# Kernel tuning notes

Hardware: AMD Instinct MI355X
Metric: run time of the kernel (lower is better)

Reference implementation:

```python
import jax, jax.numpy as jnp
import numpy as np

B, T, C = 1, 2048, 1024
H, D = 16, 64  # n_head, head_size (n_query_groups == n_head -> plain MHA)


def build_rope_cache(seq_len, n_elem, base=10000):
    theta = 1.0 / (base ** (jnp.arange(0, n_elem, 2, dtype=jnp.float32) / n_elem))
    idx_theta = jnp.outer(jnp.arange(seq_len, dtype=jnp.float32), theta)
    idx_theta = jnp.concatenate([idx_theta, idx_theta], axis=-1)  # torch .repeat(1, 2)
    return jnp.cos(idx_theta), jnp.sin(idx_theta)


def apply_rope(x, cos, sin):
    d = x.shape[-1]
    x1, x2 = x[..., : d // 2], x[..., d // 2 :]
    rotated = jnp.concatenate([-x2, x1], axis=-1)
    return x * cos + rotated * sin


def fastmax_attention(q, k, v):
    """Fastmax: first-order Taylor approx of softmax attention, causal, O(n*d^2).
    score(i,j) = 1 + q_i . k_j (temperature=1, zero RPE, no dropout);
    out_i = sum_{j<=i} score*v_j / sum_{j<=i} score, via causal cumulative sums."""
    n = q.shape[2]
    kcum = jnp.cumsum(k, axis=2)                                       # (B,H,T,D)
    kvcum = jnp.cumsum(jnp.einsum('bhnd,bhne->bhnde', k, v), axis=2)   # (B,H,T,D,D)
    den = jnp.arange(1, n + 1, dtype=q.dtype) + jnp.einsum('bhnd,bhnd->bhn', q, kcum)
    num = jnp.cumsum(v, axis=2) + jnp.einsum('bhnd,bhnde->bhne', q, kvcum)
    return num / den[..., None]


def setup_inputs() -> dict:
    key = jax.random.key(0)
    k1, k2, k3 = jax.random.split(key, 3)
    scale = 0.02
    x = jax.random.normal(k1, (B, T, C), dtype=jnp.float32)
    w_attn = jax.random.normal(k2, (3 * H * D, C), dtype=jnp.float32) * scale
    w_proj = jax.random.normal(k3, (C, H * D), dtype=jnp.float32) * scale
    cos, sin = build_rope_cache(T, D)
    return {"x": x, "w_attn": w_attn, "w_proj": w_proj, "cos": cos, "sin": sin}


def reference(x, w_attn, w_proj, cos, sin):
    Bx, Tx, Cx = x.shape
    qkv = x @ w_attn.T                                  # (B,T,3HD)
    qkv = qkv.reshape(Bx, Tx, H, 3, D).transpose(0, 2, 3, 1, 4)  # (B,H,3,T,D)
    q, k, v = qkv[:, :, 0], qkv[:, :, 1], qkv[:, :, 2]
    q = apply_rope(q, cos, sin)
    k = apply_rope(k, cos, sin)
    y = fastmax_attention(q, k, v)                      # (B,H,T,D)
    y = y.transpose(0, 2, 1, 3).reshape(Bx, Tx, H * D)
    return y @ w_proj.T
```

## Files before the change

kernel.cpp:

```cpp
#include <hip/hip_runtime.h>

#define T_LEN 2048
#define C_DIM 1024
#define H_NUM 16
#define D_DIM 64
#define QKV_N (3 * H_NUM * D_DIM)
#define L_CHK 64
#define NC (T_LEN / L_CHK)

typedef _Float16 h8 __attribute__((ext_vector_type(8)));
typedef _Float16 h4 __attribute__((ext_vector_type(4)));
typedef float f32x4 __attribute__((ext_vector_type(4)));

__global__ __launch_bounds__(256) void split3_f16(
    const float* __restrict__ x, _Float16* __restrict__ xh,
    _Float16* __restrict__ xl, const float* __restrict__ wa,
    _Float16* __restrict__ wah, _Float16* __restrict__ wal,
    const float* __restrict__ wp, _Float16* __restrict__ wph) {
  int i = (blockIdx.x * 256 + threadIdx.x) * 8;
  const float* src;
  _Float16 *dh, *dl = nullptr;
  int base;
  if (i < 2097152) {
    src = x; dh = xh; dl = xl; base = i;
  } else if (i < 2097152 + 3145728) {
    src = wa; dh = wah; dl = wal; base = i - 2097152;
  } else {
    src = wp; dh = wph; base = i - 5242880;
  }
  float4 a = *(const float4*)(src + base);
  float4 b = *(const float4*)(src + base + 4);
  float v[8] = {a.x, a.y, a.z, a.w, b.x, b.y, b.z, b.w};
  h8 hv, lv;
#pragma unroll
  for (int j = 0; j < 8; ++j) {
    float s = v[j] * 64.f;
    _Float16 h = (_Float16)s;
    hv[j] = h;
    lv[j] = (_Float16)(s - (float)h);
  }
  *(h8*)(dh + base) = hv;
  if (dl) *(h8*)(dl + base) = lv;
}

template <int BN, bool ROPE, bool SPLIT3>
__global__ __launch_bounds__(256) void gemm_nt_f16(
    const _Float16* __restrict__ Ah, const _Float16* __restrict__ Al,
    const _Float16* __restrict__ Bh, const _Float16* __restrict__ Bl,
    float* __restrict__ C, const float* __restrict__ cosb,
    const float* __restrict__ sinb, float* __restrict__ qout,
    float* __restrict__ kout, float* __restrict__ vout, int M, int N, int K,
    float outscale) {
  constexpr int NJ = BN / 32;
  constexpr int NARR = SPLIT3 ? 2 : 1;
  constexpr int GEMM_BYTES = (64 * 64 * 2 + BN * 64 * 2) * NARR;
  constexpr int ROPE_BYTES = ROPE ? (2 * 64 * 64 * 4) : 0;
  constexpr int SMEM_BYTES = GEMM_BYTES > ROPE_BYTES ? GEMM_BYTES : ROPE_BYTES;
  __shared__ __align__(16) char smem[SMEM_BYTES];
  _Float16* sAh = (_Float16*)smem;
  _Float16* sAl = sAh + 64 * 64;
  _Float16* sBh = sAh + 64 * 64 * NARR;
  _Float16* sBl = sBh + BN * 64;
  const int tid = threadIdx.x;
  const int wave = tid >> 6;
  const int lane = tid & 63;
  const int bm = blockIdx.y * 64;
  const int bn = blockIdx.x * BN;
  const int wm = wave >> 1;
  const int wn = wave & 1;
  const int srow = lane >> 3;
  const int sblk = ((lane & 7) ^ srow) * 8;
  const int quad = lane >> 4;
  const int lrow = lane & 15;

  f32x4 acc[2][NJ];
#pragma unroll
  for (int i = 0; i < 2; ++i)
#pragma unroll
    for (int j = 0; j < NJ; ++j) acc[i][j] = (f32x4){0.f, 0.f, 0.f, 0.f};

  for (int k0 = 0; k0 < K; k0 += 64) {
#pragma unroll
    for (int it = 0; it < 2; ++it) {
      const int ch = wave + it * 4;
      const int row = ch * 8 + srow;
      const _Float16* ga = Ah + (size_t)(bm + row) * K + k0 + sblk;
      __builtin_amdgcn_global_load_lds(
          (const __attribute__((address_space(1))) void*)ga,
          (__attribute__((address_space(3))) void*)(sAh + ch * 512), 16, 0, 0);
      if constexpr (SPLIT3) {
        const _Float16* gb = Al + (size_t)(bm + row) * K + k0 + sblk;
        __builtin_amdgcn_global_load_lds(
            (const __attribute__((address_space(1))) void*)gb,
            (__attribute__((address_space(3))) void*)(sAl + ch * 512), 16, 0,
            0);
      }
    }
#pragma unroll
    for (int it = 0; it < BN / 32; ++it) {
      const int ch = wave + it * 4;
      const int row = ch * 8 + srow;
      const _Float16* ga = Bh + (size_t)(bn + row) * K + k0 + sblk;
      __builtin_amdgcn_global_load_lds(
          (const __attribute__((address_space(1))) void*)ga,
          (__attribute__((address_space(3))) void*)(sBh + ch * 512), 16, 0, 0);
      if constexpr (SPLIT3) {
        const _Float16* gb = Bl + (size_t)(bn + row) * K + k0 + sblk;
        __builtin_amdgcn_global_load_lds(
            (const __attribute__((address_space(1))) void*)gb,
            (__attribute__((address_space(3))) void*)(sBl + ch * 512), 16, 0,
            0);
      }
    }
    __syncthreads();
#pragma unroll
    for (int kk = 0; kk < 2; ++kk) {
      h8 ah[2], al[2], bh[NJ], bl[NJ];
#pragma unroll
      for (int i = 0; i < 2; ++i) {
        const int row = wm * 32 + i * 16 + lrow;
        const int ra = row * 64 + (((kk * 4 + quad) ^ (row & 7)) * 8);
        ah[i] = *(const h8*)&sAh[ra];
        if constexpr (SPLIT3) al[i] = *(const h8*)&sAl[ra];
      }
#pragma unroll
      for (int j = 0; j < NJ; ++j) {
        const int row = wn * (BN / 2) + j * 16 + lrow;
        const int rb = row * 64 + (((kk * 4 + quad) ^ (row & 7)) * 8);
        bh[j] = *(const h8*)&sBh[rb];
        if constexpr (SPLIT3) bl[j] = *(const h8*)&sBl[rb];
      }
#pragma unroll
      for (int i = 0; i < 2; ++i)
#pragma unroll
        for (int j = 0; j < NJ; ++j) {
          acc[i][j] = __builtin_amdgcn_mfma_f32_16x16x32_f16(
              ah[i], bh[j], acc[i][j], 0, 0, 0);
          if constexpr (SPLIT3) {
            acc[i][j] = __builtin_amdgcn_mfma_f32_16x16x32_f16(
                ah[i], bl[j], acc[i][j], 0, 0, 0);
            acc[i][j] = __builtin_amdgcn_mfma_f32_16x16x32_f16(
                al[i], bh[j], acc[i][j], 0, 0, 0);
          }
        }
    }
    __syncthreads();
  }
  if constexpr (!ROPE) {
#pragma unroll
    for (int i = 0; i < 2; ++i) {
      const int rbase = bm + wm * 32 + i * 16 + quad * 4;
#pragma unroll
      for (int j = 0; j < NJ; ++j) {
        const int col = bn + wn * (BN / 2) + j * 16 + lrow;
#pragma unroll
        for (int r = 0; r < 4; ++r)
          C[(size_t)(rbase + r) * N + col] = acc[i][j][r] * outscale;
      }
    }
  } else {
    float* cs = (float*)smem;
    float* sn = cs + 4096;
#pragma unroll
    for (int m = 0; m < 4; ++m) {
      int el = (tid + m * 256) * 4;
      *(float4*)&cs[el] = *(const float4*)&cosb[bm * D_DIM + el];
      *(float4*)&sn[el] = *(const float4*)&sinb[bm * D_DIM + el];
    }
    __syncthreads();
    const int colbase = bn + wn * 64;
    const int type = (colbase >> 6) % 3;
    const int head = colbase / 192;
    float* dst = (type == 0) ? qout : (type == 1) ? kout : vout;
    const size_t hbase = (size_t)head * T_LEN * D_DIM;
#pragma unroll
    for (int i = 0; i < 2; ++i) {
      const int tloc0 = wm * 32 + i * 16 + quad * 4;
#pragma unroll
      for (int r = 0; r < 4; ++r) {
        const int tloc = tloc0 + r;
        float* trow = dst + hbase + (size_t)(bm + tloc) * D_DIM;
#pragma unroll
        for (int j = 0; j < NJ; ++j) {
          const int d = j * 16 + lrow;
          float val = acc[i][j][r] * outscale;
          if (type < 2) {
            float rotv = ((j < 2) ? -acc[i][j + 2][r] : acc[i][j - 2][r]) *
                         outscale;
            val = val * cs[tloc * D_DIM + d] + rotv * sn[tloc * D_DIM + d];
          }
          trow[d] = val;
        }
      }
    }
  }
}

__global__ __launch_bounds__(256) void chunk_kv(
    const float* __restrict__ k, const float* __restrict__ v,
    float* __restrict__ kvchunk, float* __restrict__ kschunk,
    float* __restrict__ vschunk) {
  __shared__ float Ks[L_CHK][D_DIM];
  __shared__ float Vs[L_CHK][D_DIM];
  int blk = blockIdx.x;
  const size_t off = ((size_t)(blk / NC) * T_LEN + (blk % NC) * L_CHK) * D_DIM;
  int tid = threadIdx.x;
#pragma unroll
  for (int m = 0; m < 4; ++m) {
    int el = (tid + m * 256) * 4;
    *(float4*)&((float*)Ks)[el] = *(const float4*)&k[off + el];
    *(float4*)&((float*)Vs)[el] = *(const float4*)&v[off + el];
  }
  __syncthreads();
  int e = tid & 63;
  int q2 = tid >> 6;
  float acc[16] = {};
  for (int t = 0; t < L_CHK; ++t) {
    float ve = Vs[t][e];
#pragma unroll
    for (int m = 0; m < 16; ++m) acc[m] += Ks[t][q2 * 16 + m] * ve;
  }
  float* outb = kvchunk + (size_t)blk * (D_DIM * D_DIM);
#pragma unroll
  for (int m = 0; m < 16; ++m) outb[(q2 * 16 + m) * D_DIM + e] = acc[m];
  if (tid < 64) {
    float s = 0.f;
    for (int t = 0; t < L_CHK; ++t) s += Ks[t][tid];
    kschunk[(size_t)blk * D_DIM + tid] = s;
  } else if (tid < 128) {
    float s = 0.f;
    for (int t = 0; t < L_CHK; ++t) s += Vs[t][tid - 64];
    vschunk[(size_t)blk * D_DIM + (tid - 64)] = s;
  }
}

__global__ __launch_bounds__(256) void scan_fused(
    const float* __restrict__ kvchunk, float* __restrict__ kvpref,
    const float* __restrict__ kschunk, const float* __restrict__ vschunk,
    float* __restrict__ kspref, float* __restrict__ vspref) {
  int b = blockIdx.x;
  int tid = threadIdx.x;
  if (b < 256) {
    int gid = b * 256 + tid;
    int h = gid >> 12;
    int de = gid & 4095;
    float vals[NC];
#pragma unroll
    for (int c = 0; c < NC; ++c)
      vals[c] = kvchunk[((size_t)(h * NC + c) << 12) + de];
    float run = 0.f;
#pragma unroll
    for (int c = 0; c < NC; ++c) {
      kvpref[((size_t)(h * NC + c) << 12) + de] = run;
      run += vals[c];
    }
  } else {
    int gid = (b - 256) * 256 + tid;
    int h = gid >> 6, d = gid & 63;
    float kv_[NC], vv_[NC];
#pragma unroll
    for (int c = 0; c < NC; ++c) {
      size_t idx = (size_t)(h * NC + c) * 64 + d;
      kv_[c] = kschunk[idx];
      vv_[c] = vschunk[idx];
    }
    float rk = 0.f, rv = 0.f;
#pragma unroll
    for (int c = 0; c < NC; ++c) {
      size_t idx = (size_t)(h * NC + c) * 64 + d;
      kspref[idx] = rk;
      vspref[idx] = rv;
      rk += kv_[c];
      rv += vv_[c];
    }
  }
}

__global__ __launch_bounds__(256) void attn_out(
    const float* __restrict__ q, const float* __restrict__ k,
    const float* __restrict__ v, const float* __restrict__ kvpref,
    const float* __restrict__ kspref, const float* __restrict__ vspref,
    _Float16* __restrict__ yh) {
  __shared__ float Ks[L_CHK * D_DIM];
  __shared__ float Vs[L_CHK * D_DIM];
  __shared__ float Ss[L_CHK][L_CHK + 1];
  int blk = blockIdx.x;
  int h = blk / NC, c = blk % NC;
  int tid = threadIdx.x;
  int r = tid & 63;
  int g = tid >> 6;
  const size_t off = ((size_t)h * T_LEN + c * L_CHK) * D_DIM;
#pragma unroll
  for (int m = 0; m < 4; ++m) {
    int el = (tid + m * 256) * 4;
    *(float4*)&Ks[el] = *(const float4*)&k[off + el];
    *(float4*)&Vs[el] = *(const float4*)&v[off + el];
  }
  float qv[D_DIM];
#pragma unroll
  for (int i = 0; i < 16; ++i) {
    float4 t4 = *(const float4*)&q[off + r * D_DIM + i * 4];
    qv[i * 4 + 0] = t4.x; qv[i * 4 + 1] = t4.y;
    qv[i * 4 + 2] = t4.z; qv[i * 4 + 3] = t4.w;
  }
  __syncthreads();
#pragma unroll
  for (int jj = 0; jj < 16; ++jj) {
    int j = g * 16 + jj;
    const float4* krow = (const float4*)&Ks[j * D_DIM];
    float sdot = 0.f;
#pragma unroll
    for (int i = 0; i < 16; ++i) {
      float4 kj = krow[i];
      sdot += qv[i * 4] * kj.x + qv[i * 4 + 1] * kj.y + qv[i * 4 + 2] * kj.z +
              qv[i * 4 + 3] * kj.w;
    }
    Ss[r][j] = (j <= r) ? (sdot + 1.f) : 0.f;
  }
  __syncthreads();
  const float* kvp = kvpref + (size_t)blk * (D_DIM * D_DIM);
#pragma unroll
  for (int m = 0; m < 4; ++m) {
    int el = (tid + m * 256) * 4;
    *(float4*)&Ks[el] = *(const float4*)&kvp[el];
  }
  __syncthreads();
  const float* ksp = kspref + (size_t)blk * D_DIM;
  const float* vsp = vspref + (size_t)blk * D_DIM;
  float den = (float)(c * L_CHK);
#pragma unroll
  for (int i = 0; i < 16; ++i) {
    float4 kk = *(const float4*)&ksp[i * 4];
    den += qv[i * 4] * kk.x + qv[i * 4 + 1] * kk.y + qv[i * 4 + 2] * kk.z +
           qv[i * 4 + 3] * kk.w;
  }
  float4 num[4];
#pragma unroll
  for (int i = 0; i < 4; ++i) num[i] = *(const float4*)&vsp[g * 16 + i * 4];
#pragma unroll
  for (int d = 0; d < D_DIM; ++d) {
    float qd = qv[d];
    const float4* kvrow = (const float4*)&Ks[d * D_DIM + g * 16];
#pragma unroll
    for (int i = 0; i < 4; ++i) {
      float4 k4 = kvrow[i];
      num[i].x += qd * k4.x; num[i].y += qd * k4.y;
      num[i].z += qd * k4.z; num[i].w += qd * k4.w;
    }
  }
  float rs = 0.f;
#pragma unroll 8
  for (int j = 0; j < L_CHK; ++j) {
    float f = Ss[r][j];
    rs += f;
    const float4* vrow = (const float4*)&Vs[j * D_DIM + g * 16];
#pragma unroll
    for (int i = 0; i < 4; ++i) {
      float4 v4 = vrow[i];
      num[i].x += f * v4.x; num[i].y += f * v4.y;
      num[i].z += f * v4.z; num[i].w += f * v4.w;
    }
  }
  den += rs;
  float inv = 1.f / den;
  int t = c * L_CHK + r;
  size_t ybase = (size_t)t * (H_NUM * D_DIM) + h * D_DIM + g * 16;
#pragma unroll
  for (int i = 0; i < 4; ++i) {
    h4 hv;
    hv[0] = (_Float16)(num[i].x * inv);
    hv[1] = (_Float16)(num[i].y * inv);
    hv[2] = (_Float16)(num[i].z * inv);
    hv[3] = (_Float16)(num[i].w * inv);
    *(h4*)&yh[ybase + i * 4] = hv;
  }
}

extern "C" void kernel_launch(void* const* d_in, const int* in_sizes, int n_in,
                              void* d_out, int out_size, void* d_ws,
                              size_t ws_size, hipStream_t stream) {
  const float* x = (const float*)d_in[0];
  const float* w_attn = (const float*)d_in[1];
  const float* w_proj = (const float*)d_in[2];
  const float* cosb = (const float*)d_in[3];
  const float* sinb = (const float*)d_in[4];
  float* out = (float*)d_out;

  char* ws = (char*)d_ws;
  float* kvchunk = (float*)ws;
  float* kvpref = (float*)(ws + 8388608);
  float* qbuf = (float*)(ws + 25165824);
  float* kbuf = (float*)(ws + 25165824 + 8388608);
  float* vbuf = (float*)(ws + 25165824 + 16777216);
  _Float16* xh = (_Float16*)(ws + 50331648);
  _Float16* xl = (_Float16*)(ws + 50331648 + 4194304);
  _Float16* yh = (_Float16*)(ws + 50331648);
  _Float16* wah = (_Float16*)(ws + 58720256);
  _Float16* wal = (_Float16*)(ws + 58720256 + 6291456);
  float* kschunk = (float*)(ws + 58720256);
  float* vschunk = (float*)(ws + 58720256 + 131072);
  float* kspref = (float*)(ws + 58720256 + 262144);
  float* vspref = (float*)(ws + 58720256 + 393216);
  _Float16* wph = (_Float16*)(ws + 71303168);

  split3_f16<<<3072, 256, 0, stream>>>(x, xh, xl, w_attn, wah, wal, w_proj,
                                       wph);

  {
    dim3 grid(QKV_N / 128, T_LEN / 64);
    gemm_nt_f16<128, true, true><<<grid, 256, 0, stream>>>(
        xh, xl, wah, wal, nullptr, cosb, sinb, qbuf, kbuf, vbuf, T_LEN, QKV_N,
        C_DIM, 1.f / 4096.f);
  }
  chunk_kv<<<H_NUM * NC, 256, 0, stream>>>(kbuf, vbuf, kvchunk, kschunk,
                                           vschunk);
  scan_fused<<<260, 256, 0, stream>>>(kvchunk, kvpref, kschunk, vschunk,
                                      kspref, vspref);
  attn_out<<<H_NUM * NC, 256, 0, stream>>>(qbuf, kbuf, vbuf, kvpref, kspref,
                                           vspref, yh);
  {
    dim3 grid(C_DIM / 64, T_LEN / 64);
    gemm_nt_f16<64, false, false><<<grid, 256, 0, stream>>>(
        yh, nullptr, wph, nullptr, out, nullptr, nullptr, nullptr, nullptr,
        nullptr, T_LEN, C_DIM, C_DIM, 1.f / 64.f);
  }
}
```

Baseline: 172.2 us.

## Fuse chunk KV, prefix scan and attention output into one flag-synchronized kernel

Merges the per-chunk K^T V computation, the cross-chunk prefix scan and the attention output into a single kernel. Each block publishes its chunk state, then sets a release flag, and later blocks spin on the flags of earlier chunks of the same head before summing their states directly. This removes two kernel launches and the kvpref round trip through global memory. In exchange, later chunks do O(c) redundant reads of earlier chunk states, and the code relies on all 512 blocks being co-resident or scheduled in order so the spin-waits cannot deadlock.

```diff
diff --git a/kernel.cpp b/kernel.cpp
--- a/kernel.cpp
+++ b/kernel.cpp
@@ -16,7 +16,15 @@
     const float* __restrict__ x, _Float16* __restrict__ xh,
     _Float16* __restrict__ xl, const float* __restrict__ wa,
     _Float16* __restrict__ wah, _Float16* __restrict__ wal,
-    const float* __restrict__ wp, _Float16* __restrict__ wph) {
+    const float* __restrict__ wp, _Float16* __restrict__ wph,
+    int* __restrict__ flags) {
+  if (blockIdx.x == 0) {
+    int t = threadIdx.x;
+    __hip_atomic_store(&flags[t], 0, __ATOMIC_RELEASE,
+                       __HIP_MEMORY_SCOPE_AGENT);
+    __hip_atomic_store(&flags[t + 256], 0, __ATOMIC_RELEASE,
+                       __HIP_MEMORY_SCOPE_AGENT);
+  }
   int i = (blockIdx.x * 256 + threadIdx.x) * 8;
   const float* src;
   _Float16 *dh, *dl = nullptr;
@@ -196,99 +204,21 @@
   }
 }
 
-__global__ __launch_bounds__(256) void chunk_kv(
-    const float* __restrict__ k, const float* __restrict__ v,
-    float* __restrict__ kvchunk, float* __restrict__ kschunk,
-    float* __restrict__ vschunk) {
-  __shared__ float Ks[L_CHK][D_DIM];
-  __shared__ float Vs[L_CHK][D_DIM];
-  int blk = blockIdx.x;
-  const size_t off = ((size_t)(blk / NC) * T_LEN + (blk % NC) * L_CHK) * D_DIM;
-  int tid = threadIdx.x;
-#pragma unroll
-  for (int m = 0; m < 4; ++m) {
-    int el = (tid + m * 256) * 4;
-    *(float4*)&((float*)Ks)[el] = *(const float4*)&k[off + el];
-    *(float4*)&((float*)Vs)[el] = *(const float4*)&v[off + el];
-  }
-  __syncthreads();
-  int e = tid & 63;
-  int q2 = tid >> 6;
-  float acc[16] = {};
-  for (int t = 0; t < L_CHK; ++t) {
-    float ve = Vs[t][e];
-#pragma unroll
-    for (int m = 0; m < 16; ++m) acc[m] += Ks[t][q2 * 16 + m] * ve;
-  }
-  float* outb = kvchunk + (size_t)blk * (D_DIM * D_DIM);
-#pragma unroll
-  for (int m = 0; m < 16; ++m) outb[(q2 * 16 + m) * D_DIM + e] = acc[m];
-  if (tid < 64) {
-    float s = 0.f;
-    for (int t = 0; t < L_CHK; ++t) s += Ks[t][tid];
-    kschunk[(size_t)blk * D_DIM + tid] = s;
-  } else if (tid < 128) {
-    float s = 0.f;
-    for (int t = 0; t < L_CHK; ++t) s += Vs[t][tid - 64];
-    vschunk[(size_t)blk * D_DIM + (tid - 64)] = s;
-  }
-}
-
-__global__ __launch_bounds__(256) void scan_fused(
-    const float* __restrict__ kvchunk, float* __restrict__ kvpref,
-    const float* __restrict__ kschunk, const float* __restrict__ vschunk,
-    float* __restrict__ kspref, float* __restrict__ vspref) {
-  int b = blockIdx.x;
-  int tid = threadIdx.x;
-  if (b < 256) {
-    int gid = b * 256 + tid;
-    int h = gid >> 12;
-    int de = gid & 4095;
-    float vals[NC];
-#pragma unroll
-    for (int c = 0; c < NC; ++c)
-      vals[c] = kvchunk[((size_t)(h * NC + c) << 12) + de];
-    float run = 0.f;
-#pragma unroll
-    for (int c = 0; c < NC; ++c) {
-      kvpref[((size_t)(h * NC + c) << 12) + de] = run;
-      run += vals[c];
-    }
-  } else {
-    int gid = (b - 256) * 256 + tid;
-    int h = gid >> 6, d = gid & 63;
-    float kv_[NC], vv_[NC];
-#pragma unroll
-    for (int c = 0; c < NC; ++c) {
-      size_t idx = (size_t)(h * NC + c) * 64 + d;
-      kv_[c] = kschunk[idx];
-      vv_[c] = vschunk[idx];
-    }
-    float rk = 0.f, rv = 0.f;
-#pragma unroll
-    for (int c = 0; c < NC; ++c) {
-      size_t idx = (size_t)(h * NC + c) * 64 + d;
-      kspref[idx] = rk;
-      vspref[idx] = rv;
-      rk += kv_[c];
-      rv += vv_[c];
-    }
-  }
-}
-
-__global__ __launch_bounds__(256) void attn_out(
+__global__ __launch_bounds__(256) void attn_fused(
     const float* __restrict__ q, const float* __restrict__ k,
-    const float* __restrict__ v, const float* __restrict__ kvpref,
-    const float* __restrict__ kspref, const float* __restrict__ vspref,
-    _Float16* __restrict__ yh) {
+    const float* __restrict__ v, float* __restrict__ kvchunk,
+    float* __restrict__ kschunk, float* __restrict__ vschunk,
+    int* __restrict__ flags, _Float16* __restrict__ yh) {
   __shared__ float Ks[L_CHK * D_DIM];
   __shared__ float Vs[L_CHK * D_DIM];
   __shared__ float Ss[L_CHK][L_CHK + 1];
-  int blk = blockIdx.x;
-  int h = blk / NC, c = blk % NC;
-  int tid = threadIdx.x;
-  int r = tid & 63;
-  int g = tid >> 6;
+  __shared__ float sKp[D_DIM];
+  __shared__ float sVp[D_DIM];
+  const int blk = blockIdx.x;
+  const int h = blk / NC, c = blk % NC;
+  const int tid = threadIdx.x;
+  const int r = tid & 63;
+  const int g = tid >> 6;
   const size_t off = ((size_t)h * T_LEN + c * L_CHK) * D_DIM;
 #pragma unroll
   for (int m = 0; m < 4; ++m) {
@@ -304,6 +234,32 @@
     qv[i * 4 + 2] = t4.z; qv[i * 4 + 3] = t4.w;
   }
   __syncthreads();
+  {
+    float agg[16] = {};
+    for (int t = 0; t < L_CHK; ++t) {
+      float ve = Vs[t * D_DIM + r];
+#pragma unroll
+      for (int m = 0; m < 16; ++m)
+        agg[m] += Ks[t * D_DIM + g * 16 + m] * ve;
+    }
+    float* outb = kvchunk + (size_t)blk * (D_DIM * D_DIM);
+#pragma unroll
+    for (int m = 0; m < 16; ++m) outb[(g * 16 + m) * D_DIM + r] = agg[m];
+    if (tid < 64) {
+      float s = 0.f;
+      for (int t = 0; t < L_CHK; ++t) s += Ks[t * D_DIM + tid];
+      kschunk[blk * D_DIM + tid] = s;
+    } else if (tid < 128) {
+      float s = 0.f;
+      for (int t = 0; t < L_CHK; ++t) s += Vs[t * D_DIM + (tid - 64)];
+      vschunk[blk * D_DIM + (tid - 64)] = s;
+    }
+  }
+  __threadfence();
+  __syncthreads();
+  if (tid == 0)
+    __hip_atomic_store(&flags[blk], 1, __ATOMIC_RELEASE,
+                       __HIP_MEMORY_SCOPE_AGENT);
 #pragma unroll
   for (int jj = 0; jj < 16; ++jj) {
     int j = g * 16 + jj;
@@ -318,25 +274,51 @@
     Ss[r][j] = (j <= r) ? (sdot + 1.f) : 0.f;
   }
   __syncthreads();
-  const float* kvp = kvpref + (size_t)blk * (D_DIM * D_DIM);
+  f32x4 pacc[4];
+#pragma unroll
+  for (int m = 0; m < 4; ++m) pacc[m] = (f32x4){0.f, 0.f, 0.f, 0.f};
+  float kp = 0.f, vp = 0.f;
+  if (c > 0) {
+    if (tid == 0) {
+      for (int cc = 0; cc < c; ++cc)
+        while (__hip_atomic_load(&flags[h * NC + cc], __ATOMIC_ACQUIRE,
+                                 __HIP_MEMORY_SCOPE_AGENT) == 0) {
+        }
+    }
+    __syncthreads();
+    for (int cc = 0; cc < c; ++cc) {
+      const float* src = kvchunk + (size_t)(h * NC + cc) * (D_DIM * D_DIM);
+#pragma unroll
+      for (int m = 0; m < 4; ++m) {
+        int el = (tid + m * 256) * 4;
+        pacc[m] += *(const f32x4*)&src[el];
+      }
+      if (tid < 64)
+        kp += kschunk[(h * NC + cc) * D_DIM + tid];
+      else if (tid < 128)
+        vp += vschunk[(h * NC + cc) * D_DIM + (tid - 64)];
+    }
+  }
 #pragma unroll
   for (int m = 0; m < 4; ++m) {
     int el = (tid + m * 256) * 4;
-    *(float4*)&Ks[el] = *(const float4*)&kvp[el];
-  }
+    *(f32x4*)&Ks[el] = pacc[m];
+  }
+  if (tid < 64)
+    sKp[tid] = kp;
+  else if (tid < 128)
+    sVp[tid - 64] = vp;
   __syncthreads();
-  const float* ksp = kspref + (size_t)blk * D_DIM;
-  const float* vsp = vspref + (size_t)blk * D_DIM;
   float den = (float)(c * L_CHK);
 #pragma unroll
   for (int i = 0; i < 16; ++i) {
-    float4 kk = *(const float4*)&ksp[i * 4];
+    const float4 kk = *(const float4*)&sKp[i * 4];
     den += qv[i * 4] * kk.x + qv[i * 4 + 1] * kk.y + qv[i * 4 + 2] * kk.z +
            qv[i * 4 + 3] * kk.w;
   }
   float4 num[4];
 #pragma unroll
-  for (int i = 0; i < 4; ++i) num[i] = *(const float4*)&vsp[g * 16 + i * 4];
+  for (int i = 0; i < 4; ++i) num[i] = *(const float4*)&sVp[g * 16 + i * 4];
 #pragma unroll
   for (int d = 0; d < D_DIM; ++d) {
     float qd = qv[d];
@@ -388,7 +370,9 @@
 
   char* ws = (char*)d_ws;
   float* kvchunk = (float*)ws;
-  float* kvpref = (float*)(ws + 8388608);
+  float* kschunk = (float*)(ws + 8388608);
+  float* vschunk = (float*)(ws + 8519680);
+  int* flags = (int*)(ws + 8650752);
   float* qbuf = (float*)(ws + 25165824);
   float* kbuf = (float*)(ws + 25165824 + 8388608);
   float* vbuf = (float*)(ws + 25165824 + 16777216);
@@ -397,14 +381,10 @@
   _Float16* yh = (_Float16*)(ws + 50331648);
   _Float16* wah = (_Float16*)(ws + 58720256);
   _Float16* wal = (_Float16*)(ws + 58720256 + 6291456);
-  float* kschunk = (float*)(ws + 58720256);
-  float* vschunk = (float*)(ws + 58720256 + 131072);
-  float* kspref = (float*)(ws + 58720256 + 262144);
-  float* vspref = (float*)(ws + 58720256 + 393216);
   _Float16* wph = (_Float16*)(ws + 71303168);
 
   split3_f16<<<3072, 256, 0, stream>>>(x, xh, xl, w_attn, wah, wal, w_proj,
-                                       wph);
+                                       wph, flags);
 
   {
     dim3 grid(QKV_N / 128, T_LEN / 64);
@@ -412,12 +392,8 @@
         xh, xl, wah, wal, nullptr, cosb, sinb, qbuf, kbuf, vbuf, T_LEN, QKV_N,
         C_DIM, 1.f / 4096.f);
   }
-  chunk_kv<<<H_NUM * NC, 256, 0, stream>>>(kbuf, vbuf, kvchunk, kschunk,
-                                           vschunk);
-  scan_fused<<<260, 256, 0, stream>>>(kvchunk, kvpref, kschunk, vschunk,
-                                      kspref, vspref);
-  attn_out<<<H_NUM * NC, 256, 0, stream>>>(qbuf, kbuf, vbuf, kvpref, kspref,
-                                           vspref, yh);
+  attn_fused<<<H_NUM * NC, 256, 0, stream>>>(qbuf, kbuf, vbuf, kvchunk,
+                                             kschunk, vschunk, flags, yh);
   {
     dim3 grid(C_DIM / 64, T_LEN / 64);
     gemm_nt_f16<64, false, false><<<grid, 256, 0, stream>>>(
```

Measured after the change: 301.4 us. 75.0% more time.
